# Performance work log

Hardware: AMD Instinct MI355X
Metric: run time of the kernel (lower is better)

The kernel has to match this reference:

```python
import jax, jax.numpy as jnp
import numpy as np

MAX_LENGTH = 10
SOS = 0
B, S, H, V = 256, 10, 1024, 32000


def setup_inputs() -> dict:
    key = jax.random.key(0)
    ks = jax.random.split(key, 16)
    p = lambda k, shp: (jax.random.normal(k, shp, dtype=jnp.float32) * 0.02)
    return {
        "encoder_outputs": jax.random.normal(ks[0], (B, S, H), dtype=jnp.float32),
        "encoder_hidden": jax.random.normal(ks[1], (1, B, H), dtype=jnp.float32),
        "target_tensor": jax.random.randint(ks[2], (B, MAX_LENGTH), 0, V),
        "emb": p(ks[3], (V, H)),
        "Wa": p(ks[4], (H, H)), "ba": p(ks[5], (H,)),
        "Ua": p(ks[6], (H, H)), "bua": p(ks[7], (H,)),
        "Va": p(ks[8], (1, H)), "bva": p(ks[9], (1,)),
        "W_ih": p(ks[10], (3 * H, 2 * H)), "W_hh": p(ks[11], (3 * H, H)),
        "b_ih": p(ks[12], (3 * H,)), "b_hh": p(ks[13], (3 * H,)),
        "W_out": p(ks[14], (V, H)), "b_out": p(ks[15], (V,)),
    }


def reference(encoder_outputs, encoder_hidden, target_tensor, emb, Wa, ba, Ua, bua,
              Va, bva, W_ih, W_hh, b_ih, b_hh, W_out, b_out):
    # Teacher forcing: input tokens are [SOS, tgt_0, ..., tgt_{T-2}]
    tokens = jnp.concatenate(
        [jnp.zeros((B, 1), dtype=target_tensor.dtype) + SOS,
         target_tensor[:, : MAX_LENGTH - 1]], axis=1)  # [B,T]
    keys = encoder_outputs                              # [B,S,H]
    keysW = jnp.einsum('bsh,oh->bso', keys, Wa) + ba    # Wa(keys), hoisted (step-invariant)

    def step(h, tok):                                   # h: [B,H], tok: [B]
        e = emb[tok]                                    # [B,H] (dropout in eval mode = identity)
        q = h @ Ua.T + bua                              # Ua(query): [B,H]
        score = jnp.tanh(keysW + q[:, None, :]) @ Va[0] + bva[0]  # [B,S]
        w = jax.nn.softmax(score, axis=1)               # softmax over seq dim
        ctx = jnp.einsum('bs,bsh->bh', w, keys)         # [B,H]
        x = jnp.concatenate([e, ctx], axis=1)           # [B,2H]
        gi = x @ W_ih.T + b_ih                          # [B,3H]
        gh = h @ W_hh.T + b_hh                          # [B,3H]
        r = jax.nn.sigmoid(gi[:, :H] + gh[:, :H])
        z = jax.nn.sigmoid(gi[:, H:2 * H] + gh[:, H:2 * H])
        n = jnp.tanh(gi[:, 2 * H:] + r * gh[:, 2 * H:])
        h_new = (1.0 - z) * n + z * h
        logits = h_new @ W_out.T + b_out                # [B,V]
        return h_new, (logits, w)

    h0 = encoder_hidden[0]                              # [B,H]
    h_last, (logits, attns) = jax.lax.scan(step, h0, tokens.T)  # logits:[T,B,V], attns:[T,B,S]
    dec_out = jax.nn.log_softmax(jnp.transpose(logits, (1, 0, 2)), axis=-1)  # [B,T,V]
    attentions = jnp.transpose(attns, (1, 0, 2)).reshape(B, MAX_LENGTH * S, 1)  # cat over dim=1
    return dec_out, h_last[None], attentions
```

## Files before the change

### kernel.cpp

```cpp
#include <hip/hip_runtime.h>
#include <hip/hip_bf16.h>
#include <math.h>

#define B_ 256
#define S_ 10
#define H_ 1024
#define V_ 32000
#define T_ 10

typedef __bf16 bf16x8 __attribute__((ext_vector_type(8)));
typedef float f32x4 __attribute__((ext_vector_type(4)));
typedef unsigned short u16;

__device__ inline u16 f2bu(float x) {
    __hip_bfloat16 b = __float2bfloat16(x);
    return *reinterpret_cast<unsigned short*>(&b);
}
__device__ inline float bu2f(u16 x) {
    unsigned u = (unsigned)x << 16;
    return __uint_as_float(u);
}

template<int BM, int BN, int BK, bool SCATTER, bool LSE, bool OUT16>
__global__ __launch_bounds__(256)
void gemm_bt(const u16* __restrict__ A, const u16* __restrict__ B,
             float* __restrict__ C, const float* __restrict__ bias,
             float* __restrict__ lse,
             int M, int N, int K, int ldc, int sb, int st)
{
    constexpr int WM = BM / 2, WN = BN / 2;
    constexpr int AT = WM / 16, BTT = WN / 16;
    constexpr int KS = BK / 32;

    constexpr int STG  = (BM + BN) * BK * 2;
    constexpr int EPI  = 4 * 16 * (WN + 4) * 4;
    constexpr int SMEM = STG > EPI ? STG : EPI;
    __shared__ __align__(16) char smem[SMEM];
    u16* As = (u16*)smem;
    u16* Bs = As + BM * BK;

    const int tid  = threadIdx.x;
    const int wave = tid >> 6;
    const int lane = tid & 63;
    const int wm   = (wave >> 1) * WM;
    const int wn   = (wave & 1) * WN;

    int id  = blockIdx.y * gridDim.x + blockIdx.x;
    int nwg = gridDim.x * gridDim.y;
    int swz = id;
    if ((nwg & 7) == 0) swz = (id & 7) * (nwg >> 3) + (id >> 3);
    const int bm = (swz % gridDim.x) * BM;
    const int bn = (swz / gridDim.x) * BN;

    const int l16 = lane & 15;
    const int lk8 = (lane >> 4) * 8;

    f32x4 acc[AT][BTT];
#pragma unroll
    for (int i = 0; i < AT; ++i)
#pragma unroll
        for (int j = 0; j < BTT; ++j) {
            f32x4 z = {0.f, 0.f, 0.f, 0.f};
            acc[i][j] = z;
        }

    constexpr int ROUNDS_A = (BM * BK) / 2048;
    constexpr int ROUNDS_B = (BN * BK) / 2048;

    for (int k0 = 0; k0 < K; k0 += BK) {
#pragma unroll
        for (int r = 0; r < ROUNDS_A; ++r) {
            int e   = r * 2048 + tid * 8;
            int row = e / BK;
            int kk  = e % BK;
            const u16* gp = A + (size_t)(bm + row) * K + k0 + kk;
            u16* lp = As + r * 2048 + wave * 512;
            __builtin_amdgcn_global_load_lds(
                (const __attribute__((address_space(1))) void*)gp,
                (__attribute__((address_space(3))) void*)lp, 16, 0, 0);
        }
        if constexpr (ROUNDS_B == 0) {
            if (tid < (BN * BK) / 8) {
                int e   = tid * 8;
                int row = e / BK;
                int kk  = e % BK;
                const u16* gp = B + (size_t)(bn + row) * K + k0 + kk;
                u16* lp = Bs + wave * 512;
                __builtin_amdgcn_global_load_lds(
                    (const __attribute__((address_space(1))) void*)gp,
                    (__attribute__((address_space(3))) void*)lp, 16, 0, 0);
            }
        } else {
#pragma unroll
            for (int r = 0; r < ROUNDS_B; ++r) {
                int e   = r * 2048 + tid * 8;
                int row = e / BK;
                int kk  = e % BK;
                const u16* gp = B + (size_t)(bn + row) * K + k0 + kk;
                u16* lp = Bs + r * 2048 + wave * 512;
                __builtin_amdgcn_global_load_lds(
                    (const __attribute__((address_space(1))) void*)gp,
                    (__attribute__((address_space(3))) void*)lp, 16, 0, 0);
            }
        }
        __syncthreads();

        bf16x8 af[KS][AT], bf[KS][BTT];
#pragma unroll
        for (int ks = 0; ks < KS; ++ks) {
#pragma unroll
            for (int i = 0; i < AT; ++i)
                af[ks][i] = *(const bf16x8*)(As + (wm + i * 16 + l16) * BK + ks * 32 + lk8);
#pragma unroll
            for (int j = 0; j < BTT; ++j)
                bf[ks][j] = *(const bf16x8*)(Bs + (wn + j * 16 + l16) * BK + ks * 32 + lk8);
        }
#pragma unroll
        for (int ks = 0; ks < KS; ++ks)
#pragma unroll
            for (int i = 0; i < AT; ++i)
#pragma unroll
                for (int j = 0; j < BTT; ++j)
                    acc[i][j] = __builtin_amdgcn_mfma_f32_16x16x32_bf16(
                        af[ks][i], bf[ks][j], acc[i][j], 0, 0, 0);
        __syncthreads();
    }

    float (*eps)[16][WN + 4] = reinterpret_cast<float (*)[16][WN + 4]>(smem);
    constexpr int C4  = WN / 4;
    constexpr int RPI = 64 / C4;
    constexpr int STEPS = 16 / RPI;
    const int chunk = lane & (C4 - 1);
    const int rg    = lane / C4;
    const int col   = bn + wn + chunk * 4;
    const int lr4   = (lane >> 4) * 4;

    f32x4 bias4 = {0.f, 0.f, 0.f, 0.f};
    if (bias) bias4 = *(const f32x4*)(bias + col);

#pragma unroll
    for (int i = 0; i < AT; ++i) {
#pragma unroll
        for (int j = 0; j < BTT; ++j)
#pragma unroll
            for (int r = 0; r < 4; ++r)
                eps[wave][lr4 + r][j * 16 + l16] = acc[i][j][r];
#pragma unroll
        for (int s = 0; s < STEPS; ++s) {
            int rowL = s * RPI + rg;
            f32x4 v = *(const f32x4*)&eps[wave][rowL][chunk * 4];
            v += bias4;
            int row = bm + wm + i * 16 + rowL;
            size_t off;
            if constexpr (SCATTER)
                off = (size_t)(row & 255) * sb + (size_t)(row >> 8) * st + col;
            else
                off = (size_t)row * ldc + col;
            if constexpr (OUT16) {
                ushort4 o = {f2bu(v[0]), f2bu(v[1]), f2bu(v[2]), f2bu(v[3])};
                *(ushort4*)((u16*)C + off) = o;
            } else if constexpr (SCATTER) {
                __builtin_nontemporal_store(v, (f32x4*)(C + off));
            } else {
                *(f32x4*)(C + off) = v;
            }
            if constexpr (LSE) {
                float es = expf(v[0]) + expf(v[1]) + expf(v[2]) + expf(v[3]);
#pragma unroll
                for (int o = C4 / 2; o > 0; o >>= 1)
                    es += __shfl_xor(es, o, 64);
                if (chunk == 0) atomicAdd(&lse[row], es);
            }
        }
    }
}

__global__ __launch_bounds__(256)
void attn_step(const float* __restrict__ keysW, const float* __restrict__ qgh,
               const float* __restrict__ Va, const float* __restrict__ bva,
               float* __restrict__ attn_out, int t)
{
    const int b = blockIdx.x;
    const int tid = threadIdx.x;
    const int lane = tid & 63, wave = tid >> 6;
    const float* qb = qgh + (size_t)b * 4096;
    const float* kW = keysW + (size_t)b * S_ * H_;

    float vh[4], qh[4];
    int hidx[4];
#pragma unroll
    for (int j = 0; j < 4; ++j) {
        int h = tid + j * 256;
        hidx[j] = h; vh[j] = Va[h]; qh[j] = qb[h];
    }

    __shared__ float lred[4][S_];
    __shared__ float wsm[S_];

#pragma unroll
    for (int s = 0; s < S_; ++s) {
        float p = 0.f;
#pragma unroll
        for (int j = 0; j < 4; ++j)
            p += vh[j] * tanhf(kW[s * H_ + hidx[j]] + qh[j]);
        for (int off = 32; off > 0; off >>= 1) p += __shfl_down(p, off, 64);
        if (lane == 0) lred[wave][s] = p;
    }
    __syncthreads();
    if (tid == 0) {
        float sc[S_], mx = -1e30f;
        for (int s = 0; s < S_; ++s) {
            sc[s] = lred[0][s] + lred[1][s] + lred[2][s] + lred[3][s] + bva[0];
            mx = fmaxf(mx, sc[s]);
        }
        float sum = 0.f;
        for (int s = 0; s < S_; ++s) { sc[s] = expf(sc[s] - mx); sum += sc[s]; }
        float inv = 1.f / sum;
        for (int s = 0; s < S_; ++s) wsm[s] = sc[s] * inv;
    }
    __syncthreads();
    if (tid < S_) attn_out[(size_t)b * 100 + t * 10 + tid] = wsm[tid];
}

__global__ __launch_bounds__(256)
void gru_fused(const float* __restrict__ qgh, const float* __restrict__ gie_t,
               const u16* __restrict__ KW2, const float* __restrict__ attnw,
               float* __restrict__ h, u16* __restrict__ Hall_t,
               float* __restrict__ hlast)
{
    const int b  = blockIdx.x;
    const int i4 = threadIdx.x * 4;

    __shared__ float ws[S_];
    if (threadIdx.x < S_) ws[threadIdx.x] = attnw[(size_t)b * 100 + threadIdx.x];
    __syncthreads();

    float ar[4] = {0,0,0,0}, az[4] = {0,0,0,0}, an[4] = {0,0,0,0};
    const u16* kwb = KW2 + (size_t)b * (S_ * 3072);
#pragma unroll
    for (int s = 0; s < S_; ++s) {
        float w = ws[s];
        const u16* kws = kwb + s * 3072;
        ushort4 vr = *(const ushort4*)(kws + i4);
        ushort4 vz = *(const ushort4*)(kws + 1024 + i4);
        ushort4 vn = *(const ushort4*)(kws + 2048 + i4);
        ar[0] += w * bu2f(vr.x); ar[1] += w * bu2f(vr.y);
        ar[2] += w * bu2f(vr.z); ar[3] += w * bu2f(vr.w);
        az[0] += w * bu2f(vz.x); az[1] += w * bu2f(vz.y);
        az[2] += w * bu2f(vz.z); az[3] += w * bu2f(vz.w);
        an[0] += w * bu2f(vn.x); an[1] += w * bu2f(vn.y);
        an[2] += w * bu2f(vn.z); an[3] += w * bu2f(vn.w);
    }

    const float* ghp = qgh + (size_t)b * 4096 + 1024;
    const float* gip = gie_t + (size_t)b * 3072;
    float4 g_r = *(const float4*)(gip + i4);
    float4 g_z = *(const float4*)(gip + 1024 + i4);
    float4 g_n = *(const float4*)(gip + 2048 + i4);
    float4 h_r = *(const float4*)(ghp + i4);
    float4 h_z = *(const float4*)(ghp + 1024 + i4);
    float4 h_n = *(const float4*)(ghp + 2048 + i4);
    float4 hold = *(const float4*)(h + (size_t)b * 1024 + i4);

    float hv[4];
#pragma unroll
    for (int r = 0; r < 4; ++r) {
        float gr = (&g_r.x)[r] + ar[r];
        float gz = (&g_z.x)[r] + az[r];
        float gn = (&g_n.x)[r] + an[r];
        float rr = 1.f / (1.f + expf(-(gr + (&h_r.x)[r])));
        float zz = 1.f / (1.f + expf(-(gz + (&h_z.x)[r])));
        float nn = tanhf(gn + rr * (&h_n.x)[r]);
        hv[r] = (1.f - zz) * nn + zz * (&hold.x)[r];
    }
    float4 hv4 = {hv[0], hv[1], hv[2], hv[3]};
    *(float4*)(h + (size_t)b * 1024 + i4) = hv4;
    ushort4 hb = {f2bu(hv[0]), f2bu(hv[1]), f2bu(hv[2]), f2bu(hv[3])};
    *(ushort4*)(Hall_t + (size_t)b * 1024 + i4) = hb;
    if (hlast) *(float4*)(hlast + (size_t)b * 1024 + i4) = hv4;
}

__global__ __launch_bounds__(256)
void lse_finish(float* __restrict__ dec, const float* __restrict__ lse)
{
    const int r = blockIdx.x;
    const int b = r & 255, t = r >> 8;
    const float l = logf(lse[r]);
    float* row = dec + (size_t)b * (T_ * V_) + (size_t)t * V_;
    for (int i = threadIdx.x * 4; i < V_; i += 1024) {
        f32x4 v = __builtin_nontemporal_load((const f32x4*)(row + i));
        v -= l;
        __builtin_nontemporal_store(v, (f32x4*)(row + i));
    }
}

__global__ __launch_bounds__(256)
void cvt_f32_bf16(const float* __restrict__ src, u16* __restrict__ dst, int n)
{
    int i = (blockIdx.x * 256 + threadIdx.x) * 4;
    float4 v = *(const float4*)(src + i);
    ushort4 o;
    o.x = f2bu(v.x); o.y = f2bu(v.y); o.z = f2bu(v.z); o.w = f2bu(v.w);
    *(ushort4*)(dst + i) = o;
}

__global__ __launch_bounds__(256)
void split_wih(const float* __restrict__ Wih, u16* __restrict__ We, u16* __restrict__ W2)
{
    int i = (blockIdx.x * 256 + threadIdx.x) * 4;
    int row = i >> 11, col = i & 2047;
    float4 v = *(const float4*)(Wih + i);
    ushort4 o;
    o.x = f2bu(v.x); o.y = f2bu(v.y); o.z = f2bu(v.z); o.w = f2bu(v.w);
    u16* dst = (col < 1024) ? (We + (size_t)row * 1024 + col)
                            : (W2 + (size_t)row * 1024 + (col - 1024));
    *(ushort4*)dst = o;
}

__global__ __launch_bounds__(256)
void build_bias1(const float* __restrict__ bua, const float* __restrict__ bhh,
                 float* __restrict__ bias1, float* __restrict__ lse)
{
    int i = blockIdx.x * 256 + threadIdx.x;
    bias1[i] = (i < 1024) ? bua[i] : bhh[i - 1024];
    if (i < 2560) lse[i] = 0.f;
}

__global__ __launch_bounds__(256)
void init_h(const float* __restrict__ eh, float* __restrict__ h, u16* __restrict__ hbf)
{
    int i = blockIdx.x * 256 + threadIdx.x;
    float v = eh[i];
    h[i] = v;
    hbf[i] = f2bu(v);
}

__global__ __launch_bounds__(256)
void gather_emb(const float* __restrict__ emb, const int* __restrict__ tgt,
                u16* __restrict__ E)
{
    int idx = blockIdx.x * 256 + threadIdx.x;
    int i4 = idx * 4;
    int m = i4 >> 10, col = i4 & 1023;
    int t = m >> 8, b = m & 255;
    int tok = (t == 0) ? 0 : tgt[b * 10 + t - 1];
    float4 v = *(const float4*)(emb + (size_t)tok * 1024 + col);
    ushort4 o;
    o.x = f2bu(v.x); o.y = f2bu(v.y); o.z = f2bu(v.z); o.w = f2bu(v.w);
    *(ushort4*)(E + (size_t)m * 1024 + col) = o;
}

extern "C" void kernel_launch(void* const* d_in, const int* in_sizes, int n_in,
                              void* d_out, int out_size, void* d_ws, size_t ws_size,
                              hipStream_t stream)
{
    const float* enc_out = (const float*)d_in[0];
    const float* enc_hid = (const float*)d_in[1];
    const int*   tgt     = (const int*)d_in[2];
    const float* emb     = (const float*)d_in[3];
    const float* Wa      = (const float*)d_in[4];
    const float* ba      = (const float*)d_in[5];
    const float* Ua      = (const float*)d_in[6];
    const float* bua     = (const float*)d_in[7];
    const float* Va      = (const float*)d_in[8];
    const float* bva     = (const float*)d_in[9];
    const float* Wih     = (const float*)d_in[10];
    const float* Whh     = (const float*)d_in[11];
    const float* bih     = (const float*)d_in[12];
    const float* bhh     = (const float*)d_in[13];
    const float* Wout    = (const float*)d_in[14];
    const float* bout    = (const float*)d_in[15];

    float* dec   = (float*)d_out;
    float* hlast = dec + (size_t)B_ * T_ * V_;
    float* attn  = hlast + (size_t)B_ * H_;

    char* ws = (char*)d_ws;
    size_t used = 0;
    auto alloc = [&](size_t bytes) {
        char* p = ws + used;
        used += (bytes + 255) & ~(size_t)255;
        return p;
    };
    u16*  Wout_b = (u16*)alloc((size_t)V_ * H_ * 2);
    u16*  Wa_b   = (u16*)alloc((size_t)H_ * H_ * 2);
    u16*  W1_b   = (u16*)alloc((size_t)4096 * H_ * 2);
    u16*  We_b   = (u16*)alloc((size_t)3072 * H_ * 2);
    u16*  W2_b   = (u16*)alloc((size_t)3072 * H_ * 2);
    u16*  keys_b = (u16*)alloc((size_t)2560 * H_ * 2);
    u16*  E_b    = (u16*)alloc((size_t)2560 * H_ * 2);
    u16*  Hall_b = (u16*)alloc((size_t)2560 * H_ * 2);
    u16*  h_b    = (u16*)alloc((size_t)B_ * H_ * 2);
    u16*  KW2    = (u16*)alloc((size_t)2560 * 3072 * 2);
    float* keysW = (float*)alloc((size_t)2560 * H_ * 4);
    float* gie   = (float*)alloc((size_t)2560 * 3072 * 4);
    float* qgh   = (float*)alloc((size_t)B_ * 4096 * 4);
    float* hbuf  = (float*)alloc((size_t)B_ * H_ * 4);
    float* bias1 = (float*)alloc(4096 * 4);
    float* lse   = (float*)alloc(2560 * 4);
    if (used > ws_size) return;

    cvt_f32_bf16<<<V_ * H_ / 1024, 256, 0, stream>>>(Wout, Wout_b, V_ * H_);
    cvt_f32_bf16<<<H_ * H_ / 1024, 256, 0, stream>>>(Wa, Wa_b, H_ * H_);
    cvt_f32_bf16<<<H_ * H_ / 1024, 256, 0, stream>>>(Ua, W1_b, H_ * H_);
    cvt_f32_bf16<<<3072 * H_ / 1024, 256, 0, stream>>>(Whh, W1_b + (size_t)1024 * H_, 3072 * H_);
    split_wih<<<3072 * 2048 / 1024, 256, 0, stream>>>(Wih, We_b, W2_b);
    cvt_f32_bf16<<<2560 * H_ / 1024, 256, 0, stream>>>(enc_out, keys_b, 2560 * H_);
    gather_emb<<<2560, 256, 0, stream>>>(emb, tgt, E_b);
    build_bias1<<<16, 256, 0, stream>>>(bua, bhh, bias1, lse);
    init_h<<<1024, 256, 0, stream>>>(enc_hid, hbuf, h_b);

    {
        dim3 g(2560 / 128, 1024 / 128);
        gemm_bt<128, 128, 32, false, false, false><<<g, 256, 0, stream>>>(
            keys_b, Wa_b, keysW, ba, nullptr, 2560, 1024, 1024, 1024, 0, 0);
    }
    {
        dim3 g(2560 / 128, 3072 / 128);
        gemm_bt<128, 128, 32, false, false, false><<<g, 256, 0, stream>>>(
            E_b, We_b, gie, bih, nullptr, 2560, 3072, 1024, 3072, 0, 0);
    }
    {
        dim3 g(2560 / 128, 3072 / 128);
        gemm_bt<128, 128, 32, false, false, true><<<g, 256, 0, stream>>>(
            keys_b, W2_b, (float*)KW2, nullptr, nullptr, 2560, 3072, 1024, 3072, 0, 0);
    }

    for (int t = 0; t < T_; ++t) {
        const u16* hsrc = (t == 0) ? h_b : (Hall_b + (size_t)(t - 1) * B_ * H_);
        {
            dim3 g(256 / 64, 4096 / 32);
            gemm_bt<64, 32, 32, false, false, false><<<g, 256, 0, stream>>>(
                hsrc, W1_b, qgh, bias1, nullptr, 256, 4096, 1024, 4096, 0, 0);
        }
        attn_step<<<256, 256, 0, stream>>>(keysW, qgh, Va, bva, attn, t);
        gru_fused<<<256, 256, 0, stream>>>(
            qgh, gie + (size_t)t * 256 * 3072, KW2, attn + (size_t)t * 10, hbuf,
            Hall_b + (size_t)t * B_ * H_, (t == T_ - 1) ? hlast : nullptr);
    }

    {
        dim3 g(2560 / 128, 32000 / 128);
        gemm_bt<128, 128, 32, true, true, false><<<g, 256, 0, stream>>>(
            Hall_b, Wout_b, dec, bout, lse, 2560, 32000, 1024,
            0, T_ * V_ , V_ );
    }
    lse_finish<<<2560, 256, 0, stream>>>(dec, lse);
}
```

Before: 1.389 ms.

## Double-buffer GEMM LDS staging and fuse attention softmax with GRU update

The GEMM main loop now uses two LDS buffers, issuing global-to-LDS loads for the next K tile before computing on the current one. This overlaps memory latency with MFMA work and replaces the two barriers per iteration with a single waitcnt plus barrier. Separately, the per-step attention kernel and GRU kernel are merged into one launch that keeps the softmax weights in shared memory, removing a launch and an attention-weight round trip in each of the ten steps. Doubling LDS use may lower occupancy for the larger tiles.

```diff
diff --git a/kernel.cpp b/kernel.cpp
--- a/kernel.cpp
+++ b/kernel.cpp
@@ -32,12 +32,12 @@
     constexpr int AT = WM / 16, BTT = WN / 16;
     constexpr int KS = BK / 32;
 
-    constexpr int STG  = (BM + BN) * BK * 2;
+    constexpr int STG  = (BM + BN) * BK;
     constexpr int EPI  = 4 * 16 * (WN + 4) * 4;
-    constexpr int SMEM = STG > EPI ? STG : EPI;
+    constexpr int SMEM = (2 * STG * 2) > EPI ? (2 * STG * 2) : EPI;
     __shared__ __align__(16) char smem[SMEM];
-    u16* As = (u16*)smem;
-    u16* Bs = As + BM * BK;
+    u16* buf0 = (u16*)smem;
+    u16* buf1 = buf0 + STG;
 
     const int tid  = threadIdx.x;
     const int wave = tid >> 6;
@@ -67,14 +67,15 @@
     constexpr int ROUNDS_A = (BM * BK) / 2048;
     constexpr int ROUNDS_B = (BN * BK) / 2048;
 
-    for (int k0 = 0; k0 < K; k0 += BK) {
+    auto stage = [&](u16* dstA, int k0) {
+        u16* dstB = dstA + BM * BK;
 #pragma unroll
         for (int r = 0; r < ROUNDS_A; ++r) {
             int e   = r * 2048 + tid * 8;
             int row = e / BK;
             int kk  = e % BK;
             const u16* gp = A + (size_t)(bm + row) * K + k0 + kk;
-            u16* lp = As + r * 2048 + wave * 512;
+            u16* lp = dstA + r * 2048 + wave * 512;
             __builtin_amdgcn_global_load_lds(
                 (const __attribute__((address_space(1))) void*)gp,
                 (__attribute__((address_space(3))) void*)lp, 16, 0, 0);
@@ -85,7 +86,7 @@
                 int row = e / BK;
                 int kk  = e % BK;
                 const u16* gp = B + (size_t)(bn + row) * K + k0 + kk;
-                u16* lp = Bs + wave * 512;
+                u16* lp = dstB + wave * 512;
                 __builtin_amdgcn_global_load_lds(
                     (const __attribute__((address_space(1))) void*)gp,
                     (__attribute__((address_space(3))) void*)lp, 16, 0, 0);
@@ -97,13 +98,24 @@
                 int row = e / BK;
                 int kk  = e % BK;
                 const u16* gp = B + (size_t)(bn + row) * K + k0 + kk;
-                u16* lp = Bs + r * 2048 + wave * 512;
+                u16* lp = dstB + r * 2048 + wave * 512;
                 __builtin_amdgcn_global_load_lds(
                     (const __attribute__((address_space(1))) void*)gp,
                     (__attribute__((address_space(3))) void*)lp, 16, 0, 0);
             }
         }
-        __syncthreads();
+    };
+
+    const int nt = K / BK;
+    stage(buf0, 0);
+    asm volatile("s_waitcnt vmcnt(0)\n\ts_barrier" ::: "memory");
+
+    int cur = 0;
+    for (int t = 0; t < nt; ++t) {
+        u16* As = cur ? buf1 : buf0;
+        u16* Bs = As + BM * BK;
+        u16* nxt = cur ? buf0 : buf1;
+        if (t + 1 < nt) stage(nxt, (t + 1) * BK);
 
         bf16x8 af[KS][AT], bf[KS][BTT];
 #pragma unroll
@@ -123,8 +135,13 @@
                 for (int j = 0; j < BTT; ++j)
                     acc[i][j] = __builtin_amdgcn_mfma_f32_16x16x32_bf16(
                         af[ks][i], bf[ks][j], acc[i][j], 0, 0, 0);
-        __syncthreads();
-    }
+
+        if (t + 1 < nt) {
+            asm volatile("s_waitcnt vmcnt(0)\n\ts_barrier" ::: "memory");
+            cur ^= 1;
+        }
+    }
+    __syncthreads();
 
     float (*eps)[16][WN + 4] = reinterpret_cast<float (*)[16][WN + 4]>(smem);
     constexpr int C4  = WN / 4;
@@ -176,9 +193,11 @@
 }
 
 __global__ __launch_bounds__(256)
-void attn_step(const float* __restrict__ keysW, const float* __restrict__ qgh,
-               const float* __restrict__ Va, const float* __restrict__ bva,
-               float* __restrict__ attn_out, int t)
+void attn_gru(const float* __restrict__ keysW, const float* __restrict__ qgh,
+              const float* __restrict__ Va, const float* __restrict__ bva,
+              const float* __restrict__ gie_t, const u16* __restrict__ KW2,
+              float* __restrict__ h, u16* __restrict__ Hall_t,
+              float* __restrict__ hlast, float* __restrict__ attn_out, int t)
 {
     const int b = blockIdx.x;
     const int tid = threadIdx.x;
@@ -187,11 +206,10 @@
     const float* kW = keysW + (size_t)b * S_ * H_;
 
     float vh[4], qh[4];
-    int hidx[4];
 #pragma unroll
     for (int j = 0; j < 4; ++j) {
-        int h = tid + j * 256;
-        hidx[j] = h; vh[j] = Va[h]; qh[j] = qb[h];
+        int hh = tid + j * 256;
+        vh[j] = Va[hh]; qh[j] = qb[hh];
     }
 
     __shared__ float lred[4][S_];
@@ -202,7 +220,7 @@
         float p = 0.f;
 #pragma unroll
         for (int j = 0; j < 4; ++j)
-            p += vh[j] * tanhf(kW[s * H_ + hidx[j]] + qh[j]);
+            p += vh[j] * tanhf(kW[s * H_ + tid + j * 256] + qh[j]);
         for (int off = 32; off > 0; off >>= 1) p += __shfl_down(p, off, 64);
         if (lane == 0) lred[wave][s] = p;
     }
@@ -220,26 +238,13 @@
     }
     __syncthreads();
     if (tid < S_) attn_out[(size_t)b * 100 + t * 10 + tid] = wsm[tid];
-}
-
-__global__ __launch_bounds__(256)
-void gru_fused(const float* __restrict__ qgh, const float* __restrict__ gie_t,
-               const u16* __restrict__ KW2, const float* __restrict__ attnw,
-               float* __restrict__ h, u16* __restrict__ Hall_t,
-               float* __restrict__ hlast)
-{
-    const int b  = blockIdx.x;
-    const int i4 = threadIdx.x * 4;
-
-    __shared__ float ws[S_];
-    if (threadIdx.x < S_) ws[threadIdx.x] = attnw[(size_t)b * 100 + threadIdx.x];
-    __syncthreads();
-
+
+    const int i4 = tid * 4;
     float ar[4] = {0,0,0,0}, az[4] = {0,0,0,0}, an[4] = {0,0,0,0};
     const u16* kwb = KW2 + (size_t)b * (S_ * 3072);
 #pragma unroll
     for (int s = 0; s < S_; ++s) {
-        float w = ws[s];
+        float w = wsm[s];
         const u16* kws = kwb + s * 3072;
         ushort4 vr = *(const ushort4*)(kws + i4);
         ushort4 vz = *(const ushort4*)(kws + 1024 + i4);
@@ -433,10 +438,10 @@
             gemm_bt<64, 32, 32, false, false, false><<<g, 256, 0, stream>>>(
                 hsrc, W1_b, qgh, bias1, nullptr, 256, 4096, 1024, 4096, 0, 0);
         }
-        attn_step<<<256, 256, 0, stream>>>(keysW, qgh, Va, bva, attn, t);
-        gru_fused<<<256, 256, 0, stream>>>(
-            qgh, gie + (size_t)t * 256 * 3072, KW2, attn + (size_t)t * 10, hbuf,
-            Hall_b + (size_t)t * B_ * H_, (t == T_ - 1) ? hlast : nullptr);
+        attn_gru<<<256, 256, 0, stream>>>(
+            keysW, qgh, Va, bva, gie + (size_t)t * 256 * 3072, KW2, hbuf,
+            Hall_b + (size_t)t * B_ * H_, (t == T_ - 1) ? hlast : nullptr,
+            attn, t);
     }
 
     {
```

After: 1.276 ms. -8.2%, faster.
